# Kernel optimization log

Hardware: AMD Instinct MI355X
Metric: run time of the kernel (lower is better)

Reference implementation:

```python
import jax, jax.numpy as jnp
import numpy as np


def setup_inputs() -> dict:
    key = jax.random.key(0)
    ks = jax.random.split(key, 9)
    B, Cr, H, W = 16, 1024, 28, 28
    Cs, Hs, Ws = 256, 25, 25  # Hs == Ws so adaptive pool == mean over width
    Ci = 512
    return {
        "x_rgb": jax.random.normal(ks[0], (B, Cr, H, W), jnp.float32),
        "x_skel": jax.random.normal(ks[1], (B, Cs, Hs, Ws), jnp.float32),
        "Wq": jax.random.normal(ks[2], (Ci, Cr), jnp.float32) * (Cr ** -0.5),
        "bq": jax.random.normal(ks[3], (Ci,), jnp.float32) * 0.01,
        "Wk": jax.random.normal(ks[4], (Ci, Cs), jnp.float32) * (Cs ** -0.5),
        "bk": jax.random.normal(ks[5], (Ci,), jnp.float32) * 0.01,
        "Wv": jax.random.normal(ks[6], (Cr, Cs), jnp.float32) * (Cs ** -0.5),
        "bv": jax.random.normal(ks[7], (Cr,), jnp.float32) * 0.01,
        "gamma": jax.random.normal(ks[8], (1,), jnp.float32) * 0.1,
    }


def reference(x_rgb, x_skel, Wq, bq, Wk, bk, Wv, bv, gamma):
    B, Cr, H, W = x_rgb.shape
    Ws = x_skel.shape[3]
    # adaptive_avg_pool2d(x_skel, (Ws, 1)) with Hs == Ws -> mean over width
    pooled = jnp.mean(x_skel, axis=3)  # [B, Cs, Ws]
    # 1x1 conv projections as matmuls
    q = jnp.einsum('ic,bchw->bihw', Wq, x_rgb) + bq[None, :, None, None]
    q = q.reshape(B, -1, H * W).transpose(0, 2, 1)          # [B, HW, Ci]
    k = jnp.einsum('ic,bcs->bis', Wk, pooled) + bk[None, :, None]  # [B, Ci, Ws]
    energy = jnp.einsum('bni,bis->bns', q, k)               # [B, HW, Ws]
    attention = jax.nn.softmax(energy, axis=-1)             # [B, HW, Ws]
    v = jnp.einsum('rc,bcs->brs', Wv, pooled) + bv[None, :, None]  # [B, Cr, Ws]
    out = jnp.einsum('brs,bns->brn', v, attention)          # [B, Cr, HW]
    out = out.reshape(B, Cr, H, W)
    return gamma[0] * out + x_rgb
```

## Files before the change

### kernel.cpp

```cpp
#include <hip/hip_runtime.h>

#define BB 16
#define CR 1024
#define HWD 784
#define HW2 392
#define CS 256
#define SSZ 25
#define SP 28
#define CI 512
#define CSPLIT 8
#define CCHUNK 128
#define RSPLIT 32
#define RCHUNK 32
#define KC 4

#define OFF_POOLED 0
#define OFF_VP     102400
#define OFF_MP     561152
#define OFF_E0     1019904
#define OFF_ATT    1020304
#define OFF_EP     1333904
#define OFF_KK     1333904
#define OFF_P      1563280

__global__ __launch_bounds__(256) void k_pool(const float* __restrict__ xs,
                                              float* __restrict__ pooled) {
    __shared__ float buf[4][400];
    int wave = threadIdx.x >> 6, lane = threadIdx.x & 63;
    int r0 = blockIdx.x * 64 + wave * 16;
    const float4* src = (const float4*)(xs + (size_t)r0 * SSZ);
    float4* b4 = (float4*)buf[wave];
    b4[lane] = src[lane];
    if (lane < 36) b4[64 + lane] = src[64 + lane];
    __syncthreads();
    if (lane < 16) {
        const float* row = buf[wave] + lane * SSZ;
        float s = 0.f;
#pragma unroll
        for (int w = 0; w < SSZ; ++w) s += row[w];
        pooled[r0 + lane] = s * (1.0f / SSZ);
    }
}

template <int NS>
__device__ __forceinline__ void proj_body(const float* __restrict__ wrow,
                                          const float* __restrict__ pb, int s0,
                                          float bias, float* __restrict__ dst,
                                          bool zpad) {
    float acc[NS];
#pragma unroll
    for (int i = 0; i < NS; ++i) acc[i] = 0.f;
    const float4* w4 = (const float4*)wrow;
#pragma unroll 4
    for (int c4 = 0; c4 < CS / 4; ++c4) {
        float4 w = w4[c4];
        const float* p = pb + c4 * 4 * SSZ + s0;
#pragma unroll
        for (int i = 0; i < NS; ++i)
            acc[i] = fmaf(w.x, p[i],
                     fmaf(w.y, p[SSZ + i],
                     fmaf(w.z, p[2 * SSZ + i],
                     fmaf(w.w, p[3 * SSZ + i], acc[i]))));
    }
#pragma unroll
    for (int i = 0; i < NS; ++i) dst[s0 + i] = acc[i] + bias;
    if (zpad) { dst[25] = 0.f; dst[26] = 0.f; dst[27] = 0.f; }
}

__global__ __launch_bounds__(256) void k_kkv(const float* __restrict__ Wk,
                                             const float* __restrict__ Wv,
                                             const float* __restrict__ bk,
                                             const float* __restrict__ bv,
                                             const float* __restrict__ pooled,
                                             float* __restrict__ kk,
                                             float* __restrict__ vp) {
    int rb = blockIdx.x >> 2, sh = blockIdx.x & 3;
    int b = blockIdx.y;
    const float* pb = pooled + (size_t)b * CS * SSZ;
    const float* wrow;
    float bias;
    float* dst;
    if (rb < 2) {
        int i = rb * 256 + threadIdx.x;
        wrow = Wk + (size_t)i * CS;
        bias = bk[i];
        dst = kk + ((size_t)b * CI + i) * SP;
    } else {
        int r = (rb - 2) * 256 + threadIdx.x;
        wrow = Wv + (size_t)r * CS;
        bias = bv[r];
        dst = vp + ((size_t)b * CR + r) * SP;
    }
    int s0 = sh * 7;
    if (sh < 3) proj_body<7>(wrow, pb, s0, bias, dst, false);
    else        proj_body<4>(wrow, pb, s0, bias, dst, true);
}

__global__ __launch_bounds__(256) void k_Mpart(const float* __restrict__ Wq,
                                               const float* __restrict__ kk,
                                               float* __restrict__ P) {
    __shared__ __align__(16) float lds[128 * 8];
    int sh = blockIdx.x, kc = blockIdx.y, b = blockIdx.z;
    int t = threadIdx.x;
    int s0 = sh * 7;
    int i0 = kc * 128;
    const float* kkb = kk + (size_t)b * CI * SP;
#pragma unroll
    for (int q = 0; q < 4; ++q) {
        int d = t + 256 * q;
        lds[d] = kkb[(size_t)(i0 + (d >> 3)) * SP + s0 + (d & 7)];
    }
    __syncthreads();

    float acc[28];
#pragma unroll
    for (int e = 0; e < 28; ++e) acc[e] = 0.f;
    const float4* lds4 = (const float4*)lds;
#pragma unroll 4
    for (int i = 0; i < 128; ++i) {
        float4 w = *(const float4*)(Wq + (size_t)(i0 + i) * CR + 4 * t);
        float4 k0 = lds4[i * 2];
        float4 k1 = lds4[i * 2 + 1];
#pragma unroll
        for (int j = 0; j < 4; ++j) {
            float wj = j == 0 ? w.x : j == 1 ? w.y : j == 2 ? w.z : w.w;
            acc[j * 7 + 0] = fmaf(wj, k0.x, acc[j * 7 + 0]);
            acc[j * 7 + 1] = fmaf(wj, k0.y, acc[j * 7 + 1]);
            acc[j * 7 + 2] = fmaf(wj, k0.z, acc[j * 7 + 2]);
            acc[j * 7 + 3] = fmaf(wj, k0.w, acc[j * 7 + 3]);
            acc[j * 7 + 4] = fmaf(wj, k1.x, acc[j * 7 + 4]);
            acc[j * 7 + 5] = fmaf(wj, k1.y, acc[j * 7 + 5]);
            acc[j * 7 + 6] = fmaf(wj, k1.z, acc[j * 7 + 6]);
        }
    }
    float* dst = P + ((((size_t)kc * BB + b) * 4 + sh) * 256 + t) * 28;
#pragma unroll
    for (int m = 0; m < 7; ++m) {
        float4 o;
        o.x = acc[4 * m + 0]; o.y = acc[4 * m + 1];
        o.z = acc[4 * m + 2]; o.w = acc[4 * m + 3];
        *(float4*)(dst + 4 * m) = o;
    }
}

__global__ __launch_bounds__(256) void k_Mred(const float* __restrict__ P,
                                              float* __restrict__ Mp) {
    int id = blockIdx.x * 256 + threadIdx.x;
    int t = id & 255, sh = (id >> 8) & 3, b = id >> 10;
    const float* p0 = P + ((((size_t)b) * 4 + sh) * 256 + t) * 28;
    const size_t PL = (size_t)BB * 4 * 256 * 28;
    float v[28];
#pragma unroll
    for (int m = 0; m < 7; ++m) {
        float4 a = *(const float4*)(p0 + 4 * m);
        float4 b1 = *(const float4*)(p0 + PL + 4 * m);
        float4 c = *(const float4*)(p0 + 2 * PL + 4 * m);
        float4 d = *(const float4*)(p0 + 3 * PL + 4 * m);
        v[4 * m + 0] = a.x + b1.x + c.x + d.x;
        v[4 * m + 1] = a.y + b1.y + c.y + d.y;
        v[4 * m + 2] = a.z + b1.z + c.z + d.z;
        v[4 * m + 3] = a.w + b1.w + c.w + d.w;
    }
    int s0 = sh * 7;
    float* mb = Mp + ((size_t)b * CR + 4 * t) * SP + s0;
#pragma unroll
    for (int j = 0; j < 4; ++j)
#pragma unroll
        for (int u = 0; u < 7; ++u)
            mb[j * SP + u] = v[j * 7 + u];
}

__global__ __launch_bounds__(64) void k_e0(const float* __restrict__ bq,
                                           const float* __restrict__ kk,
                                           float* __restrict__ e0) {
    int s = blockIdx.x, b = blockIdx.y;
    int l = threadIdx.x;
    const float* kb = kk + (size_t)b * CI * SP;
    float a = 0.f;
#pragma unroll
    for (int k = 0; k < CI / 64; ++k) {
        int i = l + 64 * k;
        a = fmaf(bq[i], kb[(size_t)i * SP + s], a);
    }
#pragma unroll
    for (int off = 32; off > 0; off >>= 1) a += __shfl_down(a, off);
    if (l == 0) e0[b * SSZ + s] = a;
}

__global__ __launch_bounds__(64) void k_energy(const float* __restrict__ xr,
                                               const float* __restrict__ Mp,
                                               float* __restrict__ Ep) {
    __shared__ float ldsM[CCHUNK * SP];
    int lane = threadIdx.x;
    int b = blockIdx.y, ch = blockIdx.z;
    int cbeg = ch * CCHUNK;
    {
        const float4* src = (const float4*)(Mp + ((size_t)b * CR + cbeg) * SP);
        float4* dst = (float4*)ldsM;
#pragma unroll
        for (int j = 0; j < 14; ++j) dst[lane + 64 * j] = src[lane + 64 * j];
    }
    __syncthreads();

    int n2 = blockIdx.x * 64 + lane;
    bool valid = n2 < HW2;
    int n2c = valid ? n2 : 0;
    const float2* x2 = (const float2*)(xr + (size_t)b * CR * HWD);

    float acc0[SP], acc1[SP];
#pragma unroll
    for (int s = 0; s < SP; ++s) { acc0[s] = 0.f; acc1[s] = 0.f; }

    for (int c = 0; c < CCHUNK; c += 4) {
        float2 xv[4];
#pragma unroll
        for (int u = 0; u < 4; ++u)
            xv[u] = x2[(size_t)(cbeg + c + u) * HW2 + n2c];
#pragma unroll
        for (int u = 0; u < 4; ++u) {
            const float4* mr = (const float4*)&ldsM[(c + u) * SP];
#pragma unroll
            for (int j = 0; j < 7; ++j) {
                float4 m = mr[j];
                acc0[4 * j + 0] = fmaf(xv[u].x, m.x, acc0[4 * j + 0]);
                acc0[4 * j + 1] = fmaf(xv[u].x, m.y, acc0[4 * j + 1]);
                acc0[4 * j + 2] = fmaf(xv[u].x, m.z, acc0[4 * j + 2]);
                acc0[4 * j + 3] = fmaf(xv[u].x, m.w, acc0[4 * j + 3]);
                acc1[4 * j + 0] = fmaf(xv[u].y, m.x, acc1[4 * j + 0]);
                acc1[4 * j + 1] = fmaf(xv[u].y, m.y, acc1[4 * j + 1]);
                acc1[4 * j + 2] = fmaf(xv[u].y, m.z, acc1[4 * j + 2]);
                acc1[4 * j + 3] = fmaf(xv[u].y, m.w, acc1[4 * j + 3]);
            }
        }
    }
    if (valid) {
        float2* ep = (float2*)Ep + ((size_t)(ch * BB + b) * SSZ) * HW2 + n2;
#pragma unroll
        for (int s = 0; s < SSZ; ++s) ep[(size_t)s * HW2] = make_float2(acc0[s], acc1[s]);
    }
}

__global__ __launch_bounds__(64) void k_softmax(const float* __restrict__ Ep,
                                                const float* __restrict__ e0,
                                                float* __restrict__ att) {
    int lane = threadIdx.x;
    int n2 = blockIdx.x * 64 + lane;
    int b = blockIdx.y;
    if (n2 >= HW2) return;
    float ex[SSZ], ey[SSZ];
#pragma unroll
    for (int s = 0; s < SSZ; ++s) { float v = e0[b * SSZ + s]; ex[s] = v; ey[s] = v; }
    const float2* ep2 = (const float2*)Ep;
    for (int ch = 0; ch < CSPLIT; ++ch) {
        const float2* ep = ep2 + ((size_t)(ch * BB + b) * SSZ) * HW2 + n2;
#pragma unroll
        for (int s = 0; s < SSZ; ++s) {
            float2 v = ep[(size_t)s * HW2];
            ex[s] += v.x; ey[s] += v.y;
        }
    }
    float mx = ex[0], my = ey[0];
#pragma unroll
    for (int s = 1; s < SSZ; ++s) { mx = fmaxf(mx, ex[s]); my = fmaxf(my, ey[s]); }
    float sx = 0.f, sy = 0.f;
#pragma unroll
    for (int s = 0; s < SSZ; ++s) {
        ex[s] = __expf(ex[s] - mx); sx += ex[s];
        ey[s] = __expf(ey[s] - my); sy += ey[s];
    }
    float ix = 1.0f / sx, iy = 1.0f / sy;
    float2* ao = (float2*)att + ((size_t)b * SSZ) * HW2 + n2;
#pragma unroll
    for (int s = 0; s < SSZ; ++s) ao[(size_t)s * HW2] = make_float2(ex[s] * ix, ey[s] * iy);
}

__global__ __launch_bounds__(64) void k_out(const float* __restrict__ xr,
                                            const float* __restrict__ vp,
                                            const float* __restrict__ att,
                                            const float* __restrict__ gamma,
                                            float* __restrict__ out) {
    __shared__ float ldsv[RCHUNK * SP];
    int lane = threadIdx.x;
    int b = blockIdx.y, rz = blockIdx.z;
    int r0 = rz * RCHUNK;
    {
        const float4* src = (const float4*)(vp + ((size_t)b * CR + r0) * SP);
        float4* dst = (float4*)ldsv;
#pragma unroll
        for (int j = 0; j < 4; ++j) {
            int idx = lane + 64 * j;
            if (idx < RCHUNK * SP / 4) dst[idx] = src[idx];
        }
    }
    __syncthreads();

    int n2 = blockIdx.x * 64 + lane;
    bool valid = n2 < HW2;
    int n2c = valid ? n2 : 0;

    float a0[SP], a1[SP];
    const float2* at2 = (const float2*)att + ((size_t)b * SSZ) * HW2 + n2c;
#pragma unroll
    for (int s = 0; s < SSZ; ++s) {
        float2 av = at2[(size_t)s * HW2];
        a0[s] = av.x; a1[s] = av.y;
    }
#pragma unroll
    for (int s = SSZ; s < SP; ++s) { a0[s] = 0.f; a1[s] = 0.f; }

    float g = gamma[0];
    const float2* x2 = (const float2*)(xr + (size_t)b * CR * HWD);
    float2* o2 = (float2*)(out + (size_t)b * CR * HWD);

#pragma unroll 4
    for (int r = 0; r < RCHUNK; ++r) {
        float2 xv = x2[(size_t)(r0 + r) * HW2 + n2c];
        float d0 = 0.f, d1 = 0.f;
        const float4* vr = (const float4*)&ldsv[r * SP];
#pragma unroll
        for (int j = 0; j < 7; ++j) {
            float4 v = vr[j];
            d0 = fmaf(v.x, a0[4 * j + 0], d0);
            d0 = fmaf(v.y, a0[4 * j + 1], d0);
            d0 = fmaf(v.z, a0[4 * j + 2], d0);
            d0 = fmaf(v.w, a0[4 * j + 3], d0);
            d1 = fmaf(v.x, a1[4 * j + 0], d1);
            d1 = fmaf(v.y, a1[4 * j + 1], d1);
            d1 = fmaf(v.z, a1[4 * j + 2], d1);
            d1 = fmaf(v.w, a1[4 * j + 3], d1);
        }
        if (valid)
            o2[(size_t)(r0 + r) * HW2 + n2] = make_float2(fmaf(g, d0, xv.x), fmaf(g, d1, xv.y));
    }
}

extern "C" void kernel_launch(void* const* d_in, const int* in_sizes, int n_in,
                              void* d_out, int out_size, void* d_ws, size_t ws_size,
                              hipStream_t stream) {
    const float* x_rgb  = (const float*)d_in[0];
    const float* x_skel = (const float*)d_in[1];
    const float* Wq     = (const float*)d_in[2];
    const float* bq     = (const float*)d_in[3];
    const float* Wk     = (const float*)d_in[4];
    const float* bk     = (const float*)d_in[5];
    const float* Wv     = (const float*)d_in[6];
    const float* bv     = (const float*)d_in[7];
    const float* gamma  = (const float*)d_in[8];
    float* out = (float*)d_out;

    float* ws     = (float*)d_ws;
    float* pooled = ws + OFF_POOLED;
    float* vp     = ws + OFF_VP;
    float* Mp     = ws + OFF_MP;
    float* e0     = ws + OFF_E0;
    float* att    = ws + OFF_ATT;
    float* Ep     = ws + OFF_EP;
    float* kk     = ws + OFF_KK;
    float* P      = ws + OFF_P;

    k_pool   <<<dim3(1600),           256, 0, stream>>>(x_skel, pooled);
    k_kkv    <<<dim3(24, 16),         256, 0, stream>>>(Wk, Wv, bk, bv, pooled, kk, vp);
    k_Mpart  <<<dim3(4, KC, 16),      256, 0, stream>>>(Wq, kk, P);
    k_Mred   <<<dim3(64),             256, 0, stream>>>(P, Mp);
    k_e0     <<<dim3(25, 16),          64, 0, stream>>>(bq, kk, e0);
    k_energy <<<dim3(7, 16, CSPLIT),   64, 0, stream>>>(x_rgb, Mp, Ep);
    k_softmax<<<dim3(7, 16),           64, 0, stream>>>(Ep, e0, att);
    k_out    <<<dim3(7, 16, RSPLIT),   64, 0, stream>>>(x_rgb, vp, att, gamma, out);
}
```

Measured before the change: 233.2 us.

## Restructure K/V projection with LDS-staged pooled input, retune Mred and energy unroll

The K/V projection kernel now stages a 4-column slice of the pooled skeleton features in LDS and has each thread compute three output rows at once, so every pooled value is reused across rows and the weights are read as float4. The grid shrinks from 24x16 to 14x16 blocks. Separately, k_Mred switches to 64-thread blocks over 256 blocks to spread the reduction across more CUs, and the energy kernel batches 8 channel loads per iteration instead of 4 to raise memory-level parallelism. The larger unroll adds register pressure in a kernel that already holds 56 accumulators.

```diff
diff --git a/kernel.cpp b/kernel.cpp
--- a/kernel.cpp
+++ b/kernel.cpp
@@ -42,31 +42,6 @@
     }
 }
 
-template <int NS>
-__device__ __forceinline__ void proj_body(const float* __restrict__ wrow,
-                                          const float* __restrict__ pb, int s0,
-                                          float bias, float* __restrict__ dst,
-                                          bool zpad) {
-    float acc[NS];
-#pragma unroll
-    for (int i = 0; i < NS; ++i) acc[i] = 0.f;
-    const float4* w4 = (const float4*)wrow;
-#pragma unroll 4
-    for (int c4 = 0; c4 < CS / 4; ++c4) {
-        float4 w = w4[c4];
-        const float* p = pb + c4 * 4 * SSZ + s0;
-#pragma unroll
-        for (int i = 0; i < NS; ++i)
-            acc[i] = fmaf(w.x, p[i],
-                     fmaf(w.y, p[SSZ + i],
-                     fmaf(w.z, p[2 * SSZ + i],
-                     fmaf(w.w, p[3 * SSZ + i], acc[i]))));
-    }
-#pragma unroll
-    for (int i = 0; i < NS; ++i) dst[s0 + i] = acc[i] + bias;
-    if (zpad) { dst[25] = 0.f; dst[26] = 0.f; dst[27] = 0.f; }
-}
-
 __global__ __launch_bounds__(256) void k_kkv(const float* __restrict__ Wk,
                                              const float* __restrict__ Wv,
                                              const float* __restrict__ bk,
@@ -74,26 +49,61 @@
                                              const float* __restrict__ pooled,
                                              float* __restrict__ kk,
                                              float* __restrict__ vp) {
-    int rb = blockIdx.x >> 2, sh = blockIdx.x & 3;
+    __shared__ __align__(16) float ldsP[4 * 256];
+    int t = threadIdx.x;
+    int rb = blockIdx.x / 7, sh = blockIdx.x % 7;
     int b = blockIdx.y;
-    const float* pb = pooled + (size_t)b * CS * SSZ;
-    const float* wrow;
-    float bias;
-    float* dst;
-    if (rb < 2) {
-        int i = rb * 256 + threadIdx.x;
-        wrow = Wk + (size_t)i * CS;
-        bias = bk[i];
-        dst = kk + ((size_t)b * CI + i) * SP;
+    int s0 = sh * 4;
+    const float* pb = pooled + (size_t)b * CS * SSZ + t * SSZ;
+#pragma unroll
+    for (int q = 0; q < 4; ++q) {
+        int s = s0 + q;
+        ldsP[q * 256 + t] = pb[s > 24 ? 24 : s];
+    }
+    __syncthreads();
+
+    int base = rb * 768;
+    int g0 = base + t, g1 = base + 256 + t, g2 = base + 512 + t;
+    const float4* w0 = (const float4*)(g0 < 512 ? Wk + (size_t)g0 * CS
+                                                : Wv + (size_t)(g0 - 512) * CS);
+    const float4* w1 = (const float4*)(g1 < 512 ? Wk + (size_t)g1 * CS
+                                                : Wv + (size_t)(g1 - 512) * CS);
+    const float4* w2 = (const float4*)(g2 < 512 ? Wk + (size_t)g2 * CS
+                                                : Wv + (size_t)(g2 - 512) * CS);
+    float acc0[4], acc1[4], acc2[4];
+#pragma unroll
+    for (int i = 0; i < 4; ++i) { acc0[i] = 0.f; acc1[i] = 0.f; acc2[i] = 0.f; }
+
+#pragma unroll 2
+    for (int c4 = 0; c4 < CS / 4; ++c4) {
+        float4 a = w0[c4], bw = w1[c4], cw = w2[c4];
+#pragma unroll
+        for (int s = 0; s < 4; ++s) {
+            float4 p = *(const float4*)&ldsP[s * 256 + 4 * c4];
+            acc0[s] = fmaf(a.x,  p.x, fmaf(a.y,  p.y, fmaf(a.z,  p.z, fmaf(a.w,  p.w, acc0[s]))));
+            acc1[s] = fmaf(bw.x, p.x, fmaf(bw.y, p.y, fmaf(bw.z, p.z, fmaf(bw.w, p.w, acc1[s]))));
+            acc2[s] = fmaf(cw.x, p.x, fmaf(cw.y, p.y, fmaf(cw.z, p.z, fmaf(cw.w, p.w, acc2[s]))));
+        }
+    }
+
+    float bias0 = g0 < 512 ? bk[g0] : bv[g0 - 512];
+    float bias1 = g1 < 512 ? bk[g1] : bv[g1 - 512];
+    float bias2 = g2 < 512 ? bk[g2] : bv[g2 - 512];
+    float* d0 = g0 < 512 ? kk + ((size_t)b * CI + g0) * SP : vp + ((size_t)b * CR + g0 - 512) * SP;
+    float* d1 = g1 < 512 ? kk + ((size_t)b * CI + g1) * SP : vp + ((size_t)b * CR + g1 - 512) * SP;
+    float* d2 = g2 < 512 ? kk + ((size_t)b * CI + g2) * SP : vp + ((size_t)b * CR + g2 - 512) * SP;
+    if (sh < 6) {
+#pragma unroll
+        for (int i = 0; i < 4; ++i) {
+            d0[s0 + i] = acc0[i] + bias0;
+            d1[s0 + i] = acc1[i] + bias1;
+            d2[s0 + i] = acc2[i] + bias2;
+        }
     } else {
-        int r = (rb - 2) * 256 + threadIdx.x;
-        wrow = Wv + (size_t)r * CS;
-        bias = bv[r];
-        dst = vp + ((size_t)b * CR + r) * SP;
-    }
-    int s0 = sh * 7;
-    if (sh < 3) proj_body<7>(wrow, pb, s0, bias, dst, false);
-    else        proj_body<4>(wrow, pb, s0, bias, dst, true);
+        d0[24] = acc0[0] + bias0; d0[25] = 0.f; d0[26] = 0.f; d0[27] = 0.f;
+        d1[24] = acc1[0] + bias1; d1[25] = 0.f; d1[26] = 0.f; d1[27] = 0.f;
+        d2[24] = acc2[0] + bias2; d2[25] = 0.f; d2[26] = 0.f; d2[27] = 0.f;
+    }
 }
 
 __global__ __launch_bounds__(256) void k_Mpart(const float* __restrict__ Wq,
@@ -143,9 +153,9 @@
     }
 }
 
-__global__ __launch_bounds__(256) void k_Mred(const float* __restrict__ P,
-                                              float* __restrict__ Mp) {
-    int id = blockIdx.x * 256 + threadIdx.x;
+__global__ __launch_bounds__(64) void k_Mred(const float* __restrict__ P,
+                                             float* __restrict__ Mp) {
+    int id = blockIdx.x * 64 + threadIdx.x;
     int t = id & 255, sh = (id >> 8) & 3, b = id >> 10;
     const float* p0 = P + ((((size_t)b) * 4 + sh) * 256 + t) * 28;
     const size_t PL = (size_t)BB * 4 * 256 * 28;
@@ -211,13 +221,13 @@
 #pragma unroll
     for (int s = 0; s < SP; ++s) { acc0[s] = 0.f; acc1[s] = 0.f; }
 
-    for (int c = 0; c < CCHUNK; c += 4) {
-        float2 xv[4];
-#pragma unroll
-        for (int u = 0; u < 4; ++u)
+    for (int c = 0; c < CCHUNK; c += 8) {
+        float2 xv[8];
+#pragma unroll
+        for (int u = 0; u < 8; ++u)
             xv[u] = x2[(size_t)(cbeg + c + u) * HW2 + n2c];
 #pragma unroll
-        for (int u = 0; u < 4; ++u) {
+        for (int u = 0; u < 8; ++u) {
             const float4* mr = (const float4*)&ldsM[(c + u) * SP];
 #pragma unroll
             for (int j = 0; j < 7; ++j) {
@@ -359,9 +369,9 @@
     float* P      = ws + OFF_P;
 
     k_pool   <<<dim3(1600),           256, 0, stream>>>(x_skel, pooled);
-    k_kkv    <<<dim3(24, 16),         256, 0, stream>>>(Wk, Wv, bk, bv, pooled, kk, vp);
+    k_kkv    <<<dim3(14, 16),         256, 0, stream>>>(Wk, Wv, bk, bv, pooled, kk, vp);
     k_Mpart  <<<dim3(4, KC, 16),      256, 0, stream>>>(Wq, kk, P);
-    k_Mred   <<<dim3(64),             256, 0, stream>>>(P, Mp);
+    k_Mred   <<<dim3(256),             64, 0, stream>>>(P, Mp);
     k_e0     <<<dim3(25, 16),          64, 0, stream>>>(bq, kk, e0);
     k_energy <<<dim3(7, 16, CSPLIT),   64, 0, stream>>>(x_rgb, Mp, Ep);
     k_softmax<<<dim3(7, 16),           64, 0, stream>>>(Ep, e0, att);
```

New measurement: 234.4 us. No clear change (+0.5%).
